# Performance work log

Hardware: AMD Instinct MI355X
Metric: run time of the kernel (lower is better)

Reference implementation:

```python
import jax, jax.numpy as jnp
import numpy as np

N_NODES = 50000


def sage_conv(x, src, dst, Wl, bl, Wr):
    # PyG SAGEConv (aggr='mean'): out = lin_l(mean_j x_j) + lin_r(x_i)
    msg = x[src]                                            # [E, d] gather
    agg = jax.ops.segment_sum(msg, dst, num_segments=N_NODES)   # [N, d]
    cnt = jax.ops.segment_sum(jnp.ones_like(dst, dtype=x.dtype), dst,
                              num_segments=N_NODES)         # [N]
    agg = agg / jnp.maximum(cnt, 1.0)[:, None]
    return agg @ Wl.T + bl + x @ Wr.T


def setup_inputs() -> dict:
    key = jax.random.key(0)
    ks = jax.random.split(key, 8)
    d = 64
    x = jax.random.normal(ks[0], (N_NODES, d), dtype=jnp.float32)
    edge_index = jax.random.randint(ks[1], (2, 800000), 0, N_NODES, dtype=jnp.int64)
    s = 1.0 / np.sqrt(d)
    Wl0 = jax.random.uniform(ks[2], (d, d), jnp.float32, -s, s)
    bl0 = jax.random.uniform(ks[3], (d,), jnp.float32, -s, s)
    Wr0 = jax.random.uniform(ks[4], (d, d), jnp.float32, -s, s)
    Wl1 = jax.random.uniform(ks[5], (d, d), jnp.float32, -s, s)
    bl1 = jax.random.uniform(ks[6], (d,), jnp.float32, -s, s)
    Wr1 = jax.random.uniform(ks[7], (d, d), jnp.float32, -s, s)
    return {"x": x, "edge_index": edge_index,
            "Wl0": Wl0, "bl0": bl0, "Wr0": Wr0,
            "Wl1": Wl1, "bl1": bl1, "Wr1": Wr1}


def reference(x, edge_index, Wl0, bl0, Wr0, Wl1, bl1, Wr1):
    src, dst = edge_index[0], edge_index[1]
    h = sage_conv(x, src, dst, Wl0, bl0, Wr0)
    h = jax.nn.relu(h)
    h = sage_conv(h, src, dst, Wl1, bl1, Wr1)
    return h
```

## Files before the change

### kernel.cpp

```cpp
#include <hip/hip_runtime.h>

#define N_NODES 50000
#define D 64
#define BKT_SHIFT 10
#define BKT_NODES 1024
#define NBKT ((N_NODES + BKT_NODES - 1) / BKT_NODES)
#define CAP 18432
#define GPAD 32
#define XBLOCKS ((N_NODES * D / 4) / 256)

typedef __attribute__((ext_vector_type(4))) float f4;
typedef __attribute__((ext_vector_type(4))) unsigned uv4;
typedef __attribute__((ext_vector_type(4))) unsigned short us4;
typedef __attribute__((ext_vector_type(8))) short bf16x8;
typedef __attribute__((ext_vector_type(4))) float f32x4;

static __device__ __forceinline__ unsigned short f2bf(float f) {
    unsigned u = __builtin_bit_cast(unsigned, f);
    unsigned r = (u + 0x7fffu + ((u >> 16) & 1u)) >> 16;
    return (unsigned short)r;
}

static __device__ __forceinline__ int detect_is64(const unsigned* __restrict__ ei32) {
    int lane = threadIdx.x & 63;
    unsigned v = (lane < 32) ? ei32[2 * lane + 1] : 0u;
    return (__ballot(v != 0u) == 0ull) ? 1 : 0;
}

static __device__ __forceinline__ int load_edges4(const unsigned* __restrict__ ei32,
                                                  int is64, int E, int base,
                                                  int* s, int* d) {
    if (base + 3 < E) {
        if (is64) {
            uv4 sa = *(const uv4*)&ei32[2 * base];
            uv4 sb = *(const uv4*)&ei32[2 * base + 4];
            uv4 da = *(const uv4*)&ei32[2 * (E + base)];
            uv4 db = *(const uv4*)&ei32[2 * (E + base) + 4];
            s[0] = (int)sa[0]; s[1] = (int)sa[2]; s[2] = (int)sb[0]; s[3] = (int)sb[2];
            d[0] = (int)da[0]; d[1] = (int)da[2]; d[2] = (int)db[0]; d[3] = (int)db[2];
        } else {
            uv4 sa = *(const uv4*)&ei32[base];
            uv4 da = *(const uv4*)&ei32[E + base];
            s[0] = (int)sa[0]; s[1] = (int)sa[1]; s[2] = (int)sa[2]; s[3] = (int)sa[3];
            d[0] = (int)da[0]; d[1] = (int)da[1]; d[2] = (int)da[2]; d[3] = (int)da[3];
        }
        return 4;
    }
    int c = 0;
    for (int e = base; e < E && e < base + 4; ++e, ++c) {
        s[c] = is64 ? (int)ei32[2 * e] : (int)ei32[e];
        d[c] = is64 ? (int)ei32[2 * (E + e)] : (int)ei32[E + e];
    }
    return c;
}

__global__ __launch_bounds__(256) void cvt_all(const float* __restrict__ x,
                                               unsigned short* __restrict__ xb,
                                               const float* __restrict__ Wl0,
                                               const float* __restrict__ Wr0,
                                               const float* __restrict__ Wl1,
                                               const float* __restrict__ Wr1,
                                               unsigned short* __restrict__ Wlb0,
                                               unsigned short* __restrict__ Wrb0,
                                               unsigned short* __restrict__ Wlb1,
                                               unsigned short* __restrict__ Wrb1,
                                               int* __restrict__ gcur) {
    int b = blockIdx.x, tid = threadIdx.x;
    if (b < XBLOCKS) {
        int i = (b * 256 + tid) * 4;
        f4 v = *(const f4*)&x[i];
        us4 o;
        o[0] = f2bf(v[0]); o[1] = f2bf(v[1]); o[2] = f2bf(v[2]); o[3] = f2bf(v[3]);
        *(us4*)&xb[i] = o;
    } else if (b < XBLOCKS + 4) {
        int w = b - XBLOCKS;
        const float* src = (w == 0) ? Wl0 : (w == 1) ? Wr0 : (w == 2) ? Wl1 : Wr1;
        unsigned short* dst = (w == 0) ? Wlb0 : (w == 1) ? Wrb0 : (w == 2) ? Wlb1 : Wrb1;
        for (int i = tid * 4; i < 64 * 64; i += 1024) {
            f4 v = *(const f4*)&src[i];
            us4 o;
            o[0] = f2bf(v[0]); o[1] = f2bf(v[1]); o[2] = f2bf(v[2]); o[3] = f2bf(v[3]);
            *(us4*)&dst[i] = o;
        }
    } else {
        if (tid < NBKT) gcur[tid * GPAD] = tid * CAP;
    }
}

__global__ __launch_bounds__(256) void bin_kernel(const unsigned* __restrict__ ei32,
                                                  int E, int* __restrict__ gcur,
                                                  unsigned* __restrict__ binned) {
    __shared__ int bc[NBKT];
    __shared__ int boff[NBKT];
    int tid = threadIdx.x;
    for (int j = tid; j < NBKT; j += 256) bc[j] = 0;
    __syncthreads();
    int is64 = detect_is64(ei32);
    int base = (blockIdx.x * 256 + tid) * 4;
    int s[4], d[4];
    int c = 0;
    if (base < E) c = load_edges4(ei32, is64, E, base, s, d);
    for (int t = 0; t < c; ++t) atomicAdd(&bc[d[t] >> BKT_SHIFT], 1);
    __syncthreads();
    for (int j = tid; j < NBKT; j += 256) {
        int v = bc[j];
        boff[j] = v ? atomicAdd(&gcur[j * GPAD], v) : 0;
        bc[j] = 0;
    }
    __syncthreads();
    for (int t = 0; t < c; ++t) {
        int bkt = d[t] >> BKT_SHIFT;
        int pos = boff[bkt] + atomicAdd(&bc[bkt], 1);
        if (pos < (bkt + 1) * CAP)
            binned[pos] = ((unsigned)(d[t] & (BKT_NODES - 1)) << 16) | (unsigned)s[t];
    }
}

__global__ __launch_bounds__(256) void build_kernel(const unsigned* __restrict__ binned,
                                                    const int* __restrict__ gcur,
                                                    int2* __restrict__ rp2,
                                                    unsigned short* __restrict__ ssrc, int n) {
    __shared__ int nc[BKT_NODES];
    __shared__ int wpart[4];
    int b = blockIdx.x;
    int tid = threadIdx.x;
    int ebase = b * CAP;
    int eend = gcur[b * GPAD];
    if (eend > (b + 1) * CAP) eend = (b + 1) * CAP;
    for (int j = tid; j < BKT_NODES; j += 256) nc[j] = 0;
    __syncthreads();
    for (int i = ebase + tid; i < eend; i += 256)
        atomicAdd(&nc[binned[i] >> 16], 1);
    __syncthreads();
    int v[4]; int ts = 0;
#pragma unroll
    for (int i = 0; i < 4; ++i) { v[i] = nc[tid * 4 + i]; ts += v[i]; }
    int lane = tid & 63, wv = tid >> 6;
    int incl = ts;
#pragma unroll
    for (int off = 1; off < 64; off <<= 1) {
        int t = __shfl_up(incl, off);
        if (lane >= off) incl += t;
    }
    if (lane == 63) wpart[wv] = incl;
    __syncthreads();
    int wb = 0;
    for (int w2 = 0; w2 < wv; ++w2) wb += wpart[w2];
    int run = ebase + wb + incl - ts;
#pragma unroll
    for (int i = 0; i < 4; ++i) {
        int node = b * BKT_NODES + tid * 4 + i;
        nc[tid * 4 + i] = run;
        if (node < n) rp2[node] = make_int2(run, v[i]);
        run += v[i];
    }
    __syncthreads();
    for (int i = ebase + tid; i < eend; i += 256) {
        unsigned u = binned[i];
        int pos = atomicAdd(&nc[u >> 16], 1);
        ssrc[pos] = (unsigned short)(u & 0xffffu);
    }
}

__global__ __launch_bounds__(256) void agg_kernel(const unsigned short* __restrict__ xb,
                                                  const int2* __restrict__ rp2,
                                                  const unsigned short* __restrict__ ssrc,
                                                  unsigned short* __restrict__ aggb, int n) {
    int gw = (blockIdx.x * 256 + threadIdx.x) >> 6;
    if (gw >= n) return;
    int lane = threadIdx.x & 63;
    int r = lane >> 3;
    int c = lane & 7;
    int2 bd = rp2[gw];
    int beg = bd.x, end = bd.x + bd.y;
    float acc[8] = {0.f, 0.f, 0.f, 0.f, 0.f, 0.f, 0.f, 0.f};
    int e = beg + r;
    for (; e + 8 < end; e += 16) {
        int s0 = ssrc[e];
        int s1 = ssrc[e + 8];
        uv4 v0 = *(const uv4*)(xb + (size_t)s0 * 64 + c * 8);
        uv4 v1 = *(const uv4*)(xb + (size_t)s1 * 64 + c * 8);
#pragma unroll
        for (int q = 0; q < 4; ++q) {
            unsigned w0 = v0[q], w1 = v1[q];
            acc[2 * q]     += __builtin_bit_cast(float, w0 << 16);
            acc[2 * q + 1] += __builtin_bit_cast(float, w0 & 0xffff0000u);
            acc[2 * q]     += __builtin_bit_cast(float, w1 << 16);
            acc[2 * q + 1] += __builtin_bit_cast(float, w1 & 0xffff0000u);
        }
    }
    if (e < end) {
        int s0 = ssrc[e];
        uv4 v0 = *(const uv4*)(xb + (size_t)s0 * 64 + c * 8);
#pragma unroll
        for (int q = 0; q < 4; ++q) {
            unsigned w0 = v0[q];
            acc[2 * q]     += __builtin_bit_cast(float, w0 << 16);
            acc[2 * q + 1] += __builtin_bit_cast(float, w0 & 0xffff0000u);
        }
    }
#pragma unroll
    for (int j = 0; j < 8; ++j) {
        float t = acc[j];
        t += __shfl_xor(t, 8);
        t += __shfl_xor(t, 16);
        t += __shfl_xor(t, 32);
        acc[j] = t;
    }
    if (r == 0) {
        int deg = bd.y;
        float inv = 1.0f / (float)(deg > 1 ? deg : 1);
        uv4 pk;
#pragma unroll
        for (int q = 0; q < 4; ++q)
            pk[q] = (unsigned)f2bf(acc[2 * q] * inv) |
                    ((unsigned)f2bf(acc[2 * q + 1] * inv) << 16);
        *(uv4*)&aggb[(size_t)gw * 64 + c * 8] = pk;
    }
}

template <bool RELU, bool LAST>
__global__ __launch_bounds__(256) void lin_mfma(const unsigned short* __restrict__ aggb,
                                                const unsigned short* __restrict__ xb,
                                                const unsigned short* __restrict__ Wlb,
                                                const float* __restrict__ bl,
                                                const unsigned short* __restrict__ Wrb,
                                                float* __restrict__ out,
                                                unsigned short* __restrict__ ob, int n) {
    int gw = (blockIdx.x * 256 + threadIdx.x) >> 6;
    int nb = gw * 16;
    if (nb >= n) return;
    int lane = threadIdx.x & 63;
    int row = lane & 15;
    int half = lane >> 4;
    int koff = half * 8;
    bf16x8 a0 = *(const bf16x8*)&aggb[(size_t)(nb + row) * 64 + koff];
    bf16x8 a1 = *(const bf16x8*)&aggb[(size_t)(nb + row) * 64 + 32 + koff];
    bf16x8 x0 = *(const bf16x8*)&xb[(size_t)(nb + row) * 64 + koff];
    bf16x8 x1 = *(const bf16x8*)&xb[(size_t)(nb + row) * 64 + 32 + koff];
    f32x4 acc[4];
#pragma unroll
    for (int ot = 0; ot < 4; ++ot) {
        int o = ot * 16 + row;
        float bv = bl[o];
        acc[ot] = (f32x4){bv, bv, bv, bv};
        bf16x8 wl0 = *(const bf16x8*)&Wlb[(size_t)o * 64 + koff];
        bf16x8 wl1 = *(const bf16x8*)&Wlb[(size_t)o * 64 + 32 + koff];
        bf16x8 wr0 = *(const bf16x8*)&Wrb[(size_t)o * 64 + koff];
        bf16x8 wr1 = *(const bf16x8*)&Wrb[(size_t)o * 64 + 32 + koff];
        acc[ot] = __builtin_amdgcn_mfma_f32_16x16x32_bf16(a0, wl0, acc[ot], 0, 0, 0);
        acc[ot] = __builtin_amdgcn_mfma_f32_16x16x32_bf16(a1, wl1, acc[ot], 0, 0, 0);
        acc[ot] = __builtin_amdgcn_mfma_f32_16x16x32_bf16(x0, wr0, acc[ot], 0, 0, 0);
        acc[ot] = __builtin_amdgcn_mfma_f32_16x16x32_bf16(x1, wr1, acc[ot], 0, 0, 0);
    }
#pragma unroll
    for (int ot = 0; ot < 4; ++ot) {
        int o = ot * 16 + row;
#pragma unroll
        for (int r = 0; r < 4; ++r) {
            float v = acc[ot][r];
            if (RELU) v = fmaxf(v, 0.f);
            int node = nb + half * 4 + r;
            if (LAST) out[(size_t)node * 64 + o] = v;
            else      ob[(size_t)node * 64 + o] = f2bf(v);
        }
    }
}

extern "C" void kernel_launch(void* const* d_in, const int* in_sizes, int n_in,
                              void* d_out, int out_size, void* d_ws, size_t ws_size,
                              hipStream_t stream) {
    const float* x      = (const float*)d_in[0];
    const unsigned* ei  = (const unsigned*)d_in[1];
    const float* Wl0    = (const float*)d_in[2];
    const float* bl0    = (const float*)d_in[3];
    const float* Wr0    = (const float*)d_in[4];
    const float* Wl1    = (const float*)d_in[5];
    const float* bl1    = (const float*)d_in[6];
    const float* Wr1    = (const float*)d_in[7];
    float* out          = (float*)d_out;

    const int N = N_NODES;
    const int E = in_sizes[1] / 2;

    char* w = (char*)d_ws;
    auto take = [&](size_t bytes) {
        char* p = w;
        w += (bytes + 255) & ~(size_t)255;
        return p;
    };
    int*            gcur   = (int*)take((size_t)NBKT * GPAD * sizeof(int));
    unsigned*       binned = (unsigned*)take((size_t)NBKT * CAP * sizeof(unsigned));
    int2*           rp2    = (int2*)take((size_t)N * sizeof(int2));
    unsigned short* ssrc   = (unsigned short*)take((size_t)NBKT * CAP * sizeof(unsigned short));
    unsigned short* xb     = (unsigned short*)take((size_t)N * D * sizeof(unsigned short));
    unsigned short* hb     = (unsigned short*)take((size_t)N * D * sizeof(unsigned short));
    unsigned short* aggb   = (unsigned short*)take((size_t)N * D * sizeof(unsigned short));
    unsigned short* Wlb0   = (unsigned short*)take((size_t)D * D * sizeof(unsigned short));
    unsigned short* Wrb0   = (unsigned short*)take((size_t)D * D * sizeof(unsigned short));
    unsigned short* Wlb1   = (unsigned short*)take((size_t)D * D * sizeof(unsigned short));
    unsigned short* Wrb1   = (unsigned short*)take((size_t)D * D * sizeof(unsigned short));

    cvt_all<<<XBLOCKS + 5, 256, 0, stream>>>(x, xb, Wl0, Wr0, Wl1, Wr1,
                                             Wlb0, Wrb0, Wlb1, Wrb1, gcur);
    int edgeBlocks = (E + 1023) / 1024;
    bin_kernel<<<edgeBlocks, 256, 0, stream>>>(ei, E, gcur, binned);
    build_kernel<<<NBKT, 256, 0, stream>>>(binned, gcur, rp2, ssrc, N);

    int aggBlocks = (N * 64 + 255) / 256;
    int linBlocks = ((N + 15) / 16 + 3) / 4;
    agg_kernel<<<aggBlocks, 256, 0, stream>>>(xb, rp2, ssrc, aggb, N);
    lin_mfma<true, false><<<linBlocks, 256, 0, stream>>>(aggb, xb, Wlb0, bl0, Wrb0,
                                                         nullptr, hb, N);
    agg_kernel<<<aggBlocks, 256, 0, stream>>>(hb, rp2, ssrc, aggb, N);
    lin_mfma<false, true><<<linBlocks, 256, 0, stream>>>(aggb, hb, Wlb1, bl1, Wrb1,
                                                         out, nullptr, N);
}
```

Before: 199.7 us.

## Fuse mean aggregation into MFMA linear kernel and widen bin/build kernels

Merges the gather-mean aggregation into the MFMA linear kernel. Each lane now accumulates the neighbours of one node for a 16-element slice and feeds the bf16 mean straight into the MFMA A operand, so the aggb intermediate and two launches go away. The cost is a different parallel mapping: 4 lanes per node instead of 64, which gives less memory-level parallelism per node and more sensitivity to degree imbalance. Separately, each bin_kernel thread now handles 8 edges, and build_kernel uses 1024 threads with one node per thread.

```diff
diff --git a/kernel.cpp b/kernel.cpp
--- a/kernel.cpp
+++ b/kernel.cpp
@@ -19,6 +19,12 @@
     unsigned u = __builtin_bit_cast(unsigned, f);
     unsigned r = (u + 0x7fffu + ((u >> 16) & 1u)) >> 16;
     return (unsigned short)r;
+}
+static __device__ __forceinline__ float bflo(unsigned w) {
+    return __builtin_bit_cast(float, w << 16);
+}
+static __device__ __forceinline__ float bfhi(unsigned w) {
+    return __builtin_bit_cast(float, w & 0xffff0000u);
 }
 
 static __device__ __forceinline__ int detect_is64(const unsigned* __restrict__ ei32) {
@@ -93,19 +99,22 @@
     __shared__ int bc[NBKT];
     __shared__ int boff[NBKT];
     int tid = threadIdx.x;
-    for (int j = tid; j < NBKT; j += 256) bc[j] = 0;
+    if (tid < NBKT) bc[tid] = 0;
     __syncthreads();
     int is64 = detect_is64(ei32);
-    int base = (blockIdx.x * 256 + tid) * 4;
-    int s[4], d[4];
+    int base = (blockIdx.x * 256 + tid) * 8;
+    int s[8], d[8];
     int c = 0;
-    if (base < E) c = load_edges4(ei32, is64, E, base, s, d);
+    if (base < E) {
+        c = load_edges4(ei32, is64, E, base, s, d);
+        if (base + 4 < E) c += load_edges4(ei32, is64, E, base + 4, s + 4, d + 4);
+    }
     for (int t = 0; t < c; ++t) atomicAdd(&bc[d[t] >> BKT_SHIFT], 1);
     __syncthreads();
-    for (int j = tid; j < NBKT; j += 256) {
-        int v = bc[j];
-        boff[j] = v ? atomicAdd(&gcur[j * GPAD], v) : 0;
-        bc[j] = 0;
+    if (tid < NBKT) {
+        int v = bc[tid];
+        boff[tid] = v ? atomicAdd(&gcur[tid * GPAD], v) : 0;
+        bc[tid] = 0;
     }
     __syncthreads();
     for (int t = 0; t < c; ++t) {
@@ -116,27 +125,25 @@
     }
 }
 
-__global__ __launch_bounds__(256) void build_kernel(const unsigned* __restrict__ binned,
-                                                    const int* __restrict__ gcur,
-                                                    int2* __restrict__ rp2,
-                                                    unsigned short* __restrict__ ssrc, int n) {
+__global__ __launch_bounds__(1024) void build_kernel(const unsigned* __restrict__ binned,
+                                                     const int* __restrict__ gcur,
+                                                     int2* __restrict__ rp2,
+                                                     unsigned short* __restrict__ ssrc, int n) {
     __shared__ int nc[BKT_NODES];
-    __shared__ int wpart[4];
+    __shared__ int wpart[16];
     int b = blockIdx.x;
     int tid = threadIdx.x;
     int ebase = b * CAP;
     int eend = gcur[b * GPAD];
-    if (eend > (b + 1) * CAP) eend = (b + 1) * CAP;
-    for (int j = tid; j < BKT_NODES; j += 256) nc[j] = 0;
-    __syncthreads();
-    for (int i = ebase + tid; i < eend; i += 256)
+    if (eend > ebase + CAP) eend = ebase + CAP;
+    nc[tid] = 0;
+    __syncthreads();
+    for (int i = ebase + tid; i < eend; i += 1024)
         atomicAdd(&nc[binned[i] >> 16], 1);
     __syncthreads();
-    int v[4]; int ts = 0;
-#pragma unroll
-    for (int i = 0; i < 4; ++i) { v[i] = nc[tid * 4 + i]; ts += v[i]; }
+    int v = nc[tid];
     int lane = tid & 63, wv = tid >> 6;
-    int incl = ts;
+    int incl = v;
 #pragma unroll
     for (int off = 1; off < 64; off <<= 1) {
         int t = __shfl_up(incl, off);
@@ -144,89 +151,29 @@
     }
     if (lane == 63) wpart[wv] = incl;
     __syncthreads();
-    int wb = 0;
-    for (int w2 = 0; w2 < wv; ++w2) wb += wpart[w2];
-    int run = ebase + wb + incl - ts;
-#pragma unroll
-    for (int i = 0; i < 4; ++i) {
-        int node = b * BKT_NODES + tid * 4 + i;
-        nc[tid * 4 + i] = run;
-        if (node < n) rp2[node] = make_int2(run, v[i]);
-        run += v[i];
-    }
-    __syncthreads();
-    for (int i = ebase + tid; i < eend; i += 256) {
+    int pre = 0;
+    for (int w2 = 0; w2 < wv; ++w2) pre += wpart[w2];
+    int run = ebase + pre + incl - v;
+    int node = b * BKT_NODES + tid;
+    nc[tid] = run;
+    if (node < n) rp2[node] = make_int2(run, v);
+    __syncthreads();
+    for (int i = ebase + tid; i < eend; i += 1024) {
         unsigned u = binned[i];
         int pos = atomicAdd(&nc[u >> 16], 1);
         ssrc[pos] = (unsigned short)(u & 0xffffu);
     }
 }
 
-__global__ __launch_bounds__(256) void agg_kernel(const unsigned short* __restrict__ xb,
+template <bool RELU, bool LAST>
+__global__ __launch_bounds__(256) void sage_fused(const unsigned short* __restrict__ xb,
                                                   const int2* __restrict__ rp2,
                                                   const unsigned short* __restrict__ ssrc,
-                                                  unsigned short* __restrict__ aggb, int n) {
-    int gw = (blockIdx.x * 256 + threadIdx.x) >> 6;
-    if (gw >= n) return;
-    int lane = threadIdx.x & 63;
-    int r = lane >> 3;
-    int c = lane & 7;
-    int2 bd = rp2[gw];
-    int beg = bd.x, end = bd.x + bd.y;
-    float acc[8] = {0.f, 0.f, 0.f, 0.f, 0.f, 0.f, 0.f, 0.f};
-    int e = beg + r;
-    for (; e + 8 < end; e += 16) {
-        int s0 = ssrc[e];
-        int s1 = ssrc[e + 8];
-        uv4 v0 = *(const uv4*)(xb + (size_t)s0 * 64 + c * 8);
-        uv4 v1 = *(const uv4*)(xb + (size_t)s1 * 64 + c * 8);
-#pragma unroll
-        for (int q = 0; q < 4; ++q) {
-            unsigned w0 = v0[q], w1 = v1[q];
-            acc[2 * q]     += __builtin_bit_cast(float, w0 << 16);
-            acc[2 * q + 1] += __builtin_bit_cast(float, w0 & 0xffff0000u);
-            acc[2 * q]     += __builtin_bit_cast(float, w1 << 16);
-            acc[2 * q + 1] += __builtin_bit_cast(float, w1 & 0xffff0000u);
-        }
-    }
-    if (e < end) {
-        int s0 = ssrc[e];
-        uv4 v0 = *(const uv4*)(xb + (size_t)s0 * 64 + c * 8);
-#pragma unroll
-        for (int q = 0; q < 4; ++q) {
-            unsigned w0 = v0[q];
-            acc[2 * q]     += __builtin_bit_cast(float, w0 << 16);
-            acc[2 * q + 1] += __builtin_bit_cast(float, w0 & 0xffff0000u);
-        }
-    }
-#pragma unroll
-    for (int j = 0; j < 8; ++j) {
-        float t = acc[j];
-        t += __shfl_xor(t, 8);
-        t += __shfl_xor(t, 16);
-        t += __shfl_xor(t, 32);
-        acc[j] = t;
-    }
-    if (r == 0) {
-        int deg = bd.y;
-        float inv = 1.0f / (float)(deg > 1 ? deg : 1);
-        uv4 pk;
-#pragma unroll
-        for (int q = 0; q < 4; ++q)
-            pk[q] = (unsigned)f2bf(acc[2 * q] * inv) |
-                    ((unsigned)f2bf(acc[2 * q + 1] * inv) << 16);
-        *(uv4*)&aggb[(size_t)gw * 64 + c * 8] = pk;
-    }
-}
-
-template <bool RELU, bool LAST>
-__global__ __launch_bounds__(256) void lin_mfma(const unsigned short* __restrict__ aggb,
-                                                const unsigned short* __restrict__ xb,
-                                                const unsigned short* __restrict__ Wlb,
-                                                const float* __restrict__ bl,
-                                                const unsigned short* __restrict__ Wrb,
-                                                float* __restrict__ out,
-                                                unsigned short* __restrict__ ob, int n) {
+                                                  const unsigned short* __restrict__ Wlb,
+                                                  const float* __restrict__ bl,
+                                                  const unsigned short* __restrict__ Wrb,
+                                                  float* __restrict__ out,
+                                                  unsigned short* __restrict__ ob, int n) {
     int gw = (blockIdx.x * 256 + threadIdx.x) >> 6;
     int nb = gw * 16;
     if (nb >= n) return;
@@ -234,35 +181,81 @@
     int row = lane & 15;
     int half = lane >> 4;
     int koff = half * 8;
-    bf16x8 a0 = *(const bf16x8*)&aggb[(size_t)(nb + row) * 64 + koff];
-    bf16x8 a1 = *(const bf16x8*)&aggb[(size_t)(nb + row) * 64 + 32 + koff];
-    bf16x8 x0 = *(const bf16x8*)&xb[(size_t)(nb + row) * 64 + koff];
-    bf16x8 x1 = *(const bf16x8*)&xb[(size_t)(nb + row) * 64 + 32 + koff];
-    f32x4 acc[4];
+    int node = nb + row;
+    int2 bd = rp2[node];
+    int beg = bd.x, end = bd.x + bd.y;
+
+    float acc[16];
+#pragma unroll
+    for (int j = 0; j < 16; ++j) acc[j] = 0.f;
+
+    int e = beg;
+    for (; e + 1 < end; e += 2) {
+        int s0 = ssrc[e], s1 = ssrc[e + 1];
+        uv4 v0 = *(const uv4*)(xb + (size_t)s0 * 64 + koff);
+        uv4 v1 = *(const uv4*)(xb + (size_t)s0 * 64 + 32 + koff);
+        uv4 v2 = *(const uv4*)(xb + (size_t)s1 * 64 + koff);
+        uv4 v3 = *(const uv4*)(xb + (size_t)s1 * 64 + 32 + koff);
+#pragma unroll
+        for (int q = 0; q < 4; ++q) {
+            acc[2 * q]     += bflo(v0[q]) + bflo(v2[q]);
+            acc[2 * q + 1] += bfhi(v0[q]) + bfhi(v2[q]);
+            acc[8 + 2 * q]     += bflo(v1[q]) + bflo(v3[q]);
+            acc[8 + 2 * q + 1] += bfhi(v1[q]) + bfhi(v3[q]);
+        }
+    }
+    if (e < end) {
+        int s0 = ssrc[e];
+        uv4 v0 = *(const uv4*)(xb + (size_t)s0 * 64 + koff);
+        uv4 v1 = *(const uv4*)(xb + (size_t)s0 * 64 + 32 + koff);
+#pragma unroll
+        for (int q = 0; q < 4; ++q) {
+            acc[2 * q]     += bflo(v0[q]);
+            acc[2 * q + 1] += bfhi(v0[q]);
+            acc[8 + 2 * q]     += bflo(v1[q]);
+            acc[8 + 2 * q + 1] += bfhi(v1[q]);
+        }
+    }
+
+    float inv = 1.0f / (float)(bd.y > 1 ? bd.y : 1);
+    uv4 pa0, pa1;
+#pragma unroll
+    for (int q = 0; q < 4; ++q) {
+        pa0[q] = (unsigned)f2bf(acc[2 * q] * inv) |
+                 ((unsigned)f2bf(acc[2 * q + 1] * inv) << 16);
+        pa1[q] = (unsigned)f2bf(acc[8 + 2 * q] * inv) |
+                 ((unsigned)f2bf(acc[8 + 2 * q + 1] * inv) << 16);
+    }
+    bf16x8 a0 = __builtin_bit_cast(bf16x8, pa0);
+    bf16x8 a1 = __builtin_bit_cast(bf16x8, pa1);
+    bf16x8 x0 = *(const bf16x8*)&xb[(size_t)node * 64 + koff];
+    bf16x8 x1 = *(const bf16x8*)&xb[(size_t)node * 64 + 32 + koff];
+
+    f32x4 accd[4];
 #pragma unroll
     for (int ot = 0; ot < 4; ++ot) {
         int o = ot * 16 + row;
         float bv = bl[o];
-        acc[ot] = (f32x4){bv, bv, bv, bv};
+        accd[ot] = (f32x4){bv, bv, bv, bv};
         bf16x8 wl0 = *(const bf16x8*)&Wlb[(size_t)o * 64 + koff];
         bf16x8 wl1 = *(const bf16x8*)&Wlb[(size_t)o * 64 + 32 + koff];
         bf16x8 wr0 = *(const bf16x8*)&Wrb[(size_t)o * 64 + koff];
         bf16x8 wr1 = *(const bf16x8*)&Wrb[(size_t)o * 64 + 32 + koff];
-        acc[ot] = __builtin_amdgcn_mfma_f32_16x16x32_bf16(a0, wl0, acc[ot], 0, 0, 0);
-        acc[ot] = __builtin_amdgcn_mfma_f32_16x16x32_bf16(a1, wl1, acc[ot], 0, 0, 0);
-        acc[ot] = __builtin_amdgcn_mfma_f32_16x16x32_bf16(x0, wr0, acc[ot], 0, 0, 0);
-        acc[ot] = __builtin_amdgcn_mfma_f32_16x16x32_bf16(x1, wr1, acc[ot], 0, 0, 0);
+        accd[ot] = __builtin_amdgcn_mfma_f32_16x16x32_bf16(a0, wl0, accd[ot], 0, 0, 0);
+        accd[ot] = __builtin_amdgcn_mfma_f32_16x16x32_bf16(a1, wl1, accd[ot], 0, 0, 0);
+        accd[ot] = __builtin_amdgcn_mfma_f32_16x16x32_bf16(x0, wr0, accd[ot], 0, 0, 0);
+        accd[ot] = __builtin_amdgcn_mfma_f32_16x16x32_bf16(x1, wr1, accd[ot], 0, 0, 0);
     }
 #pragma unroll
     for (int ot = 0; ot < 4; ++ot) {
         int o = ot * 16 + row;
 #pragma unroll
         for (int r = 0; r < 4; ++r) {
-            float v = acc[ot][r];
+            float v = accd[ot][r];
             if (RELU) v = fmaxf(v, 0.f);
-            int node = nb + half * 4 + r;
-            if (LAST) out[(size_t)node * 64 + o] = v;
-            else      ob[(size_t)node * 64 + o] = f2bf(v);
+            int nd = nb + half * 4 + r;
+            if (LAST) out[(size_t)nd * 64 + o] = v;
+            else      ob[(size_t)nd * 64 + o] = f2bf(v);
         }
     }
 }
@@ -295,7 +288,6 @@
     unsigned short* ssrc   = (unsigned short*)take((size_t)NBKT * CAP * sizeof(unsigned short));
     unsigned short* xb     = (unsigned short*)take((size_t)N * D * sizeof(unsigned short));
     unsigned short* hb     = (unsigned short*)take((size_t)N * D * sizeof(unsigned short));
-    unsigned short* aggb   = (unsigned short*)take((size_t)N * D * sizeof(unsigned short));
     unsigned short* Wlb0   = (unsigned short*)take((size_t)D * D * sizeof(unsigned short));
     unsigned short* Wrb0   = (unsigned short*)take((size_t)D * D * sizeof(unsigned short));
     unsigned short* Wlb1   = (unsigned short*)take((size_t)D * D * sizeof(unsigned short));
@@ -303,16 +295,13 @@
 
     cvt_all<<<XBLOCKS + 5, 256, 0, stream>>>(x, xb, Wl0, Wr0, Wl1, Wr1,
                                              Wlb0, Wrb0, Wlb1, Wrb1, gcur);
-    int edgeBlocks = (E + 1023) / 1024;
+    int edgeBlocks = (E + 2047) / 2048;
     bin_kernel<<<edgeBlocks, 256, 0, stream>>>(ei, E, gcur, binned);
-    build_kernel<<<NBKT, 256, 0, stream>>>(binned, gcur, rp2, ssrc, N);
-
-    int aggBlocks = (N * 64 + 255) / 256;
-    int linBlocks = ((N + 15) / 16 + 3) / 4;
-    agg_kernel<<<aggBlocks, 256, 0, stream>>>(xb, rp2, ssrc, aggb, N);
-    lin_mfma<true, false><<<linBlocks, 256, 0, stream>>>(aggb, xb, Wlb0, bl0, Wrb0,
-                                                         nullptr, hb, N);
-    agg_kernel<<<aggBlocks, 256, 0, stream>>>(hb, rp2, ssrc, aggb, N);
-    lin_mfma<false, true><<<linBlocks, 256, 0, stream>>>(aggb, hb, Wlb1, bl1, Wrb1,
-                                                         out, nullptr, N);
-}
+    build_kernel<<<NBKT, 1024, 0, stream>>>(binned, gcur, rp2, ssrc, N);
+
+    int fusedBlocks = (N + 63) / 64;
+    sage_fused<true, false><<<fusedBlocks, 256, 0, stream>>>(xb, rp2, ssrc, Wlb0, bl0, Wrb0,
+                                                             nullptr, hb, N);
+    sage_fused<false, true><<<fusedBlocks, 256, 0, stream>>>(hb, rp2, ssrc, Wlb1, bl1, Wrb1,
+                                                             out, nullptr, N);
+}
```

Result: faster. 169.7 us (-15.0%).
